# Performance work log

Hardware: AMD Instinct MI355X
Metric: run time of the kernel (lower is better)

## Reference

```python
import jax, jax.numpy as jnp
import numpy as np

VOCAB, EMB, HID, LAT, LAYERS = 32000, 512, 1024, 1024, 2
B, T = 16, 128
IN0 = EMB + HID          # layer-0 GRU input size (emb concat syn_z)
OUT_IN = HID + LAT + EMB # out-projection input (use_last_output=True)


def gru_cell(x, h, W_ih, W_hh, b_ih, b_hh):
    # PyTorch GRUCell: gates ordered [r, z, n]
    gi = x @ W_ih.T + b_ih
    gh = h @ W_hh.T + b_hh
    i_r, i_z, i_n = jnp.split(gi, 3, axis=-1)
    h_r, h_z, h_n = jnp.split(gh, 3, axis=-1)
    r = jax.nn.sigmoid(i_r + h_r)
    z = jax.nn.sigmoid(i_z + h_z)
    n = jnp.tanh(i_n + r * h_n)
    return (1.0 - z) * n + z * h


def setup_inputs() -> dict:
    key = jax.random.key(0)
    ks = jax.random.split(key, 16)
    s = 0.02
    return {
        "input_seq": jax.random.randint(ks[0], (B, T), 0, VOCAB),
        "prev_output": jnp.zeros((B, HID), jnp.float32),
        "sem_z": jax.random.normal(ks[1], (B, LAT), jnp.float32),
        "syn_z": jax.random.normal(ks[2], (B, HID), jnp.float32),
        "hidden": jnp.zeros((LAYERS, B, HID), jnp.float32),
        "emb_table": jax.random.normal(ks[3], (VOCAB, EMB), jnp.float32) * s,
        "W_ih0": jax.random.normal(ks[4], (3 * HID, IN0), jnp.float32) * s,
        "W_hh0": jax.random.normal(ks[5], (3 * HID, HID), jnp.float32) * s,
        "b_ih0": jnp.zeros((3 * HID,), jnp.float32),
        "b_hh0": jnp.zeros((3 * HID,), jnp.float32),
        "W_ih1": jax.random.normal(ks[6], (3 * HID, HID), jnp.float32) * s,
        "W_hh1": jax.random.normal(ks[7], (3 * HID, HID), jnp.float32) * s,
        "b_ih1": jnp.zeros((3 * HID,), jnp.float32),
        "b_hh1": jnp.zeros((3 * HID,), jnp.float32),
        "W_out": jax.random.normal(ks[8], (VOCAB, OUT_IN), jnp.float32) * s,
        "b_out": jnp.zeros((VOCAB,), jnp.float32),
    }


def reference(input_seq, prev_output, sem_z, syn_z, hidden, emb_table,
              W_ih0, W_hh0, b_ih0, b_hh0, W_ih1, W_hh1, b_ih1, b_hh1,
              W_out, b_out):
    # dropout=0.0 -> identity; input_feeding=False so prev_output is unused.
    embs = emb_table[input_seq]            # [B, T, E]
    embs_t = jnp.swapaxes(embs, 0, 1)      # [T, B, E]

    def step(h, emb_t):
        x = jnp.concatenate([emb_t, syn_z], axis=1)        # [B, E+H]
        h0 = gru_cell(x, h[0], W_ih0, W_hh0, b_ih0, b_hh0)  # [B, H]
        h1 = gru_cell(h0, h[1], W_ih1, W_hh1, b_ih1, b_hh1)
        pred = jnp.concatenate([h1, sem_z, emb_t], axis=1)  # [B, H+L+E]
        logits = pred @ W_out.T + b_out                     # [B, V]
        scores = jax.nn.log_softmax(logits, axis=-1)
        return jnp.stack([h0, h1]), (scores, logits)

    hidden_f, (scores, logits) = jax.lax.scan(step, hidden, embs_t)
    # scores/logits: [T, B, V]; output = last layer hidden at final step
    return scores, hidden_f, hidden_f[-1], logits
```

## Files before the change

kernel.cpp:

```cpp
#include <hip/hip_runtime.h>

typedef unsigned short u16;
typedef __attribute__((ext_vector_type(8))) short bf16x8;
typedef __attribute__((ext_vector_type(4))) float f32x4;

__device__ __forceinline__ float bf2f(u16 u) {
  union { unsigned u; float f; } v; v.u = ((unsigned)u) << 16; return v.f;
}
__device__ __forceinline__ u16 f2bf(float f) {
  union { float f; unsigned u; } v; v.f = f;
  unsigned r = v.u + 0x7FFFu + ((v.u >> 16) & 1u);
  return (u16)(r >> 16);
}

__device__ __forceinline__ f32x4 ld_sc_x4(const u16* p) {
  f32x4 r;
  asm volatile("global_load_dwordx4 %0, %1, off sc0 sc1"
               : "=v"(r) : "v"(p) : "memory");
  return r;
}
__device__ __forceinline__ float ld_sc_f32(const float* p) {
  float r;
  asm volatile("global_load_dword %0, %1, off sc0 sc1"
               : "=v"(r) : "v"(p) : "memory");
  return r;
}
__device__ __forceinline__ void st_sc_u16(u16* p, unsigned v) {
  asm volatile("global_store_short %0, %1, off sc0 sc1"
               :: "v"(p), "v"(v) : "memory");
}
__device__ __forceinline__ void st_sc_f32(float* p, float v) {
  asm volatile("global_store_dword %0, %1, off sc0 sc1"
               :: "v"(p), "v"(v) : "memory");
}
#define WAIT_VM0() asm volatile("s_waitcnt vmcnt(0)" ::: "memory")

__device__ __forceinline__ int ld_flag(const int* p) {
  return __hip_atomic_load(p, __ATOMIC_RELAXED, __HIP_MEMORY_SCOPE_AGENT);
}
__device__ __forceinline__ void st_flag(int* p, int v) {
  __hip_atomic_store(p, v, __ATOMIC_RELAXED, __HIP_MEMORY_SCOPE_AGENT);
}

constexpr size_t OFF_WCAT  = 0;
constexpr size_t OFF_WSEM  = 98304000;
constexpr size_t OFF_PART  = 98304000;
constexpr size_t OFF_H1ALL = 130000000;
constexpr size_t OFF_GI0   = 163840000;
constexpr size_t OFF_XOUT  = 189005824;
constexpr size_t OFF_H0ALL = 195297280;
constexpr size_t OFF_WIH0E = 199491584;
constexpr size_t OFF_WIH0S = 202637312;
constexpr size_t OFF_WHH0  = 208928768;
constexpr size_t OFF_WIH1  = 215220224;
constexpr size_t OFF_WHH1  = 221511680;
constexpr size_t OFF_SYNB  = 227803136;
constexpr size_t OFF_SEMB  = 228065280;
constexpr size_t OFF_BASE0 = 228327424;
constexpr size_t OFF_BASEO = 229900288;
constexpr size_t OFF_H0IBF = 246284288;
constexpr size_t OFF_H1IBF = 246317056;
constexpr size_t OFF_FLAGS = 246349824;
constexpr size_t OFF_HIDF  = 262144000;
constexpr size_t OFF_LAST  = 262275072;
constexpr size_t OFF_LOGIT = 262340608;

__global__ __launch_bounds__(256) void conv_bf16_k(
    const float* __restrict__ src, u16* __restrict__ dst,
    int rows, int cols8, int sld, int soff, int dld, int doff) {
  int t = blockIdx.x * 256 + threadIdx.x;
  if (t >= rows * cols8) return;
  int r = t / cols8, c = (t - r * cols8) * 8;
  const float* s = src + (size_t)r * sld + soff + c;
  float4 a = *(const float4*)s;
  float4 b = *(const float4*)(s + 4);
  bf16x8 o;
  o[0] = (short)f2bf(a.x); o[1] = (short)f2bf(a.y);
  o[2] = (short)f2bf(a.z); o[3] = (short)f2bf(a.w);
  o[4] = (short)f2bf(b.x); o[5] = (short)f2bf(b.y);
  o[6] = (short)f2bf(b.z); o[7] = (short)f2bf(b.w);
  *(bf16x8*)(dst + (size_t)r * dld + doff + c) = o;
}

__global__ __launch_bounds__(256) void pack_pad_bf16_k(
    const float* __restrict__ src, u16* __restrict__ dst) {
  int t = blockIdx.x * 256 + threadIdx.x;
  int row = t >> 7, c = (t & 127) * 8;
  bf16x8 o = {0, 0, 0, 0, 0, 0, 0, 0};
  if (row < 16) {
    const float* s = src + row * 1024 + c;
    float4 a = *(const float4*)s;
    float4 b = *(const float4*)(s + 4);
    o[0] = (short)f2bf(a.x); o[1] = (short)f2bf(a.y);
    o[2] = (short)f2bf(a.z); o[3] = (short)f2bf(a.w);
    o[4] = (short)f2bf(b.x); o[5] = (short)f2bf(b.y);
    o[6] = (short)f2bf(b.z); o[7] = (short)f2bf(b.w);
  }
  *(bf16x8*)(dst + (size_t)row * 1024 + c) = o;
}

__global__ __launch_bounds__(256) void gather_emb_k(
    const int* __restrict__ seq, const float* __restrict__ table,
    u16* __restrict__ xout) {
  int t0 = blockIdx.x * 256 + threadIdx.x;
  int tb = t0 >> 6, c = (t0 & 63) * 8;
  int tt = tb >> 4, b = tb & 15;
  int tok = seq[b * 128 + tt];
  const float* s = table + (size_t)tok * 512 + c;
  float4 a = *(const float4*)s;
  float4 bb = *(const float4*)(s + 4);
  bf16x8 o;
  o[0] = (short)f2bf(a.x);  o[1] = (short)f2bf(a.y);
  o[2] = (short)f2bf(a.z);  o[3] = (short)f2bf(a.w);
  o[4] = (short)f2bf(bb.x); o[5] = (short)f2bf(bb.y);
  o[6] = (short)f2bf(bb.z); o[7] = (short)f2bf(bb.w);
  *(bf16x8*)(xout + (size_t)tb * 1536 + 1024 + c) = o;
}

__global__ __launch_bounds__(256) void init_h_k(
    const float* __restrict__ hidden, u16* __restrict__ h0b,
    u16* __restrict__ h1b, int* __restrict__ flags) {
  int i = blockIdx.x * 256 + threadIdx.x;
  h0b[i] = f2bf(hidden[i]);
  h1b[i] = f2bf(hidden[16384 + i]);
  if (i < 4096) flags[i] = 0;
}

__device__ __forceinline__ void stage_tile(const u16* src, char* tile,
                                           int tid) {
  f32x4 tmp[8];
#pragma unroll
  for (int q = 0; q < 8; ++q) {
    int c = q * 256 + tid;
    int row = c >> 7, kc = c & 127;
    tmp[q] = ld_sc_x4(src + (size_t)row * 1024 + kc * 8);
  }
  WAIT_VM0();
#pragma unroll
  for (int q = 0; q < 8; ++q) {
    int c = q * 256 + tid;
    int row = c >> 7, kc = c & 127;
    int byte = (row * 2048 + kc * 16) ^ ((row & 7) << 4);
    *(bf16x8*)(tile + byte) = *(bf16x8*)&tmp[q];
  }
}

__global__ __launch_bounds__(256, 1) void gru_persist3_k(
    const float* __restrict__ hidden, const u16* __restrict__ h0i,
    const u16* __restrict__ h1i, const float* __restrict__ gi0,
    const u16* __restrict__ Whh0, const u16* __restrict__ Wih1,
    const u16* __restrict__ Whh1, const float* __restrict__ bhh0,
    const float* __restrict__ bih1, const float* __restrict__ bhh1,
    u16* __restrict__ h0all, u16* __restrict__ h1all, u16* __restrict__ xout,
    float* __restrict__ part, float* __restrict__ hidf,
    float* __restrict__ last, int* __restrict__ flags) {
  extern __shared__ char ldsb[];
  char* Ab = ldsb + 98304;
  float* Cl = (float*)(ldsb + 131072);
  const int tid = threadIdx.x, bid = blockIdx.x;
  const int wave = tid >> 6, lane = tid & 63;
  const int role = bid >> 6, lb = bid & 63, jb = lb * 16;
  int* f0 = flags, *fih = flags + 1024, *f1 = flags + 2048;

  const u16* Wsrc = role == 0 ? Whh0 : (role == 1 ? Wih1 : Whh1);
  for (int idx = tid; idx < 48 * 128; idx += 256) {
    int row = idx >> 7, c = idx & 127;
    int g = row >> 4, jj = row & 15;
    const u16* src = Wsrc + (size_t)(g * 1024 + jb + jj) * 1024 + c * 8;
    int byte = (row * 2048 + c * 16) ^ ((row & 7) << 4);
    *(bf16x8*)(ldsb + byte) = *(const bf16x8*)src;
  }

  const int eb = tid >> 4, jj = tid & 15, j = jb + jj;
  float hp = 0.f, bR = 0.f, bZ = 0.f, bN = 0.f, iR = 0.f, iZ = 0.f, iN = 0.f;
  if (role == 0) {
    hp = hidden[eb * 1024 + j];
    bR = bhh0[j]; bZ = bhh0[1024 + j]; bN = bhh0[2048 + j];
  } else if (role == 2) {
    hp = hidden[16384 + eb * 1024 + j];
    bR = bhh1[j]; bZ = bhh1[1024 + j]; bN = bhh1[2048 + j];
    iR = bih1[j]; iZ = bih1[1024 + j]; iN = bih1[2048 + j];
  }
  __syncthreads();

  const int arow = lane & 15, aq = lane >> 4;
  for (int t = 0; t < 128; ++t) {
    if (role == 0) {
      if (t > 0 && tid < 64)
        while (ld_flag(f0 + tid * 16) < t) __builtin_amdgcn_s_sleep(1);
    } else if (role == 1) {
      if (tid < 64)
        while (ld_flag(f0 + tid * 16) < t + 1) __builtin_amdgcn_s_sleep(1);
    } else {
      if (t > 0 && tid < 64)
        while (ld_flag(f1 + tid * 16) < t) __builtin_amdgcn_s_sleep(1);
    }
    __syncthreads();

    const u16* asrc;
    if (role == 0)      asrc = t ? h0all + (size_t)(t - 1) * 16384 : h0i;
    else if (role == 1) asrc = h0all + (size_t)t * 16384;
    else                asrc = t ? h1all + (size_t)(t - 1) * 16384 : h1i;
    stage_tile(asrc, Ab, tid);
    __syncthreads();

    {
      f32x4 a0 = {0.f, 0.f, 0.f, 0.f}, a1 = a0, a2 = a0;
#pragma unroll
      for (int i = 0; i < 8; ++i) {
        int ks = wave + i * 4;
        int abyte = (arow * 2048 + ks * 64 + aq * 16) ^ ((arow & 7) << 4);
        bf16x8 af = *(const bf16x8*)(Ab + abyte);
        int r0 = arow, r1 = 16 + arow, r2 = 32 + arow;
        bf16x8 b0 = *(const bf16x8*)(
            ldsb + ((r0 * 2048 + ks * 64 + aq * 16) ^ ((r0 & 7) << 4)));
        bf16x8 b1 = *(const bf16x8*)(
            ldsb + ((r1 * 2048 + ks * 64 + aq * 16) ^ ((r1 & 7) << 4)));
        bf16x8 b2 = *(const bf16x8*)(
            ldsb + ((r2 * 2048 + ks * 64 + aq * 16) ^ ((r2 & 7) << 4)));
        a0 = __builtin_amdgcn_mfma_f32_16x16x32_bf16(af, b0, a0, 0, 0, 0);
        a1 = __builtin_amdgcn_mfma_f32_16x16x32_bf16(af, b1, a1, 0, 0, 0);
        a2 = __builtin_amdgcn_mfma_f32_16x16x32_bf16(af, b2, a2, 0, 0, 0);
      }
#pragma unroll
      for (int r = 0; r < 4; ++r) {
        int ci = (aq * 4 + r) * 16 + arow;
        Cl[(0 * 4 + wave) * 256 + ci] = a0[r];
        Cl[(1 * 4 + wave) * 256 + ci] = a1[r];
        Cl[(2 * 4 + wave) * 256 + ci] = a2[r];
      }
    }
    if (role == 2 && tid == 0)
      while (ld_flag(fih + lb * 16) < t + 1) __builtin_amdgcn_s_sleep(1);
    __syncthreads();

    {
      int ci = eb * 16 + jj;
      float s0 = Cl[(0 * 4 + 0) * 256 + ci] + Cl[(0 * 4 + 1) * 256 + ci] +
                 Cl[(0 * 4 + 2) * 256 + ci] + Cl[(0 * 4 + 3) * 256 + ci];
      float s1 = Cl[(1 * 4 + 0) * 256 + ci] + Cl[(1 * 4 + 1) * 256 + ci] +
                 Cl[(1 * 4 + 2) * 256 + ci] + Cl[(1 * 4 + 3) * 256 + ci];
      float s2 = Cl[(2 * 4 + 0) * 256 + ci] + Cl[(2 * 4 + 1) * 256 + ci] +
                 Cl[(2 * 4 + 2) * 256 + ci] + Cl[(2 * 4 + 3) * 256 + ci];
      if (role == 1) {
        float* pp = part + ((size_t)t * 64 + lb) * 768 + eb * 16 + jj;
        st_sc_f32(pp, s0);
        st_sc_f32(pp + 256, s1);
        st_sc_f32(pp + 512, s2);
        WAIT_VM0();
      } else {
        float ir, iz, inn;
        if (role == 0) {
          const float* g = gi0 + ((size_t)t * 16 + eb) * 3072 + j;
          ir = g[0]; iz = g[1024]; inn = g[2048];
        } else {
          const float* pp = part + ((size_t)t * 64 + lb) * 768 + eb * 16 + jj;
          float p0 = ld_sc_f32(pp), p1 = ld_sc_f32(pp + 256),
                p2 = ld_sc_f32(pp + 512);
          WAIT_VM0();
          ir = p0 + iR; iz = p1 + iZ; inn = p2 + iN;
        }
        float r = 1.f / (1.f + __expf(-(ir + s0 + bR)));
        float z = 1.f / (1.f + __expf(-(iz + s1 + bZ)));
        float n = tanhf(inn + r * (s2 + bN));
        float hnew = (1.f - z) * n + z * hp;
        hp = hnew;
        u16 hb = f2bf(hnew);
        if (role == 0) {
          st_sc_u16(h0all + ((size_t)t * 16 + eb) * 1024 + j, (unsigned)hb);
          if (t == 127) hidf[eb * 1024 + j] = hnew;
        } else {
          st_sc_u16(h1all + ((size_t)t * 16 + eb) * 1024 + j, (unsigned)hb);
          xout[((size_t)t * 16 + eb) * 1536 + j] = hb;
          if (t == 127) {
            hidf[16384 + eb * 1024 + j] = hnew;
            last[eb * 1024 + j] = hnew;
          }
        }
        WAIT_VM0();
      }
    }
    __syncthreads();
    if (tid == 0) {
      if (role == 0)      st_flag(f0 + lb * 16, t + 1);
      else if (role == 1) st_flag(fih + lb * 16, t + 1);
      else                st_flag(f1 + lb * 16, t + 1);
    }
  }
}

template <int MODE>
__global__ __launch_bounds__(256) void gemm_bt_k(
    const u16* __restrict__ A, int lda, const u16* __restrict__ Bw, int ldb,
    float* __restrict__ C, int ldc, const float* __restrict__ add,
    int N, int K) {
  __shared__ u16 Asm_[128 * 32];
  __shared__ u16 Bsm_[128 * 32];
  const int m0 = blockIdx.x * 128, n0 = blockIdx.y * 128;
  const int tid = threadIdx.x, wave = tid >> 6, lane = tid & 63;
  const int wm = (wave >> 1) * 64, wn = (wave & 1) * 64;
  const int lrow = lane & 15, lk = (lane >> 4) * 8;
  f32x4 acc[4][4] = {};
  for (int k0 = 0; k0 < K; k0 += 32) {
    __syncthreads();
#pragma unroll
    for (int q = 0; q < 2; ++q) {
      int c = (wave * 2 + q) * 64 + lane;
      int row = c >> 2, seg = c & 3;
      const u16* src = A + (size_t)(m0 + row) * lda + k0 + seg * 8;
      u16* dst = Asm_ + (wave * 2 + q) * 512;
      __builtin_amdgcn_global_load_lds(
          (const __attribute__((address_space(1))) void*)src,
          (__attribute__((address_space(3))) void*)dst, 16, 0, 0);
    }
#pragma unroll
    for (int q = 0; q < 2; ++q) {
      int c = (wave * 2 + q) * 64 + lane;
      int row = c >> 2, seg = c & 3;
      const u16* src = Bw + (size_t)(n0 + row) * ldb + k0 + seg * 8;
      u16* dst = Bsm_ + (wave * 2 + q) * 512;
      __builtin_amdgcn_global_load_lds(
          (const __attribute__((address_space(1))) void*)src,
          (__attribute__((address_space(3))) void*)dst, 16, 0, 0);
    }
    asm volatile("s_waitcnt vmcnt(0)" ::: "memory");
    __syncthreads();
    bf16x8 af[4], bfr[4];
#pragma unroll
    for (int i = 0; i < 4; ++i) {
      af[i]  = *(const bf16x8*)(Asm_ + (wm + i * 16 + lrow) * 32 + lk);
      bfr[i] = *(const bf16x8*)(Bsm_ + (wn + i * 16 + lrow) * 32 + lk);
    }
#pragma unroll
    for (int i = 0; i < 4; ++i)
#pragma unroll
      for (int j = 0; j < 4; ++j)
        acc[i][j] = __builtin_amdgcn_mfma_f32_16x16x32_bf16(
            af[i], bfr[j], acc[i][j], 0, 0, 0);
  }
  const int lr4 = (lane >> 4) * 4;
#pragma unroll
  for (int i = 0; i < 4; ++i) {
#pragma unroll
    for (int j = 0; j < 4; ++j) {
      int gc = n0 + wn + j * 16 + lrow;
#pragma unroll
      for (int r = 0; r < 4; ++r) {
        int gr = m0 + wm + i * 16 + lr4 + r;
        float v = acc[i][j][r];
        if (MODE == 1) v += add[(gr & 15) * N + gc];
        else if (MODE == 2) v += add[gc];
        C[(size_t)gr * ldc + gc] = v;
      }
    }
  }
}

__global__ __launch_bounds__(256) void log_softmax_k(
    const float* __restrict__ logits, float* __restrict__ scores) {
  int row = blockIdx.x;
  const float* x = logits + (size_t)row * 32000;
  float* y = scores + (size_t)row * 32000;
  __shared__ float red[8];
  int tid = threadIdx.x;
  float m = -3.4e38f;
  for (int idx = tid * 4; idx < 32000; idx += 1024) {
    float4 v = *(const float4*)(x + idx);
    m = fmaxf(m, fmaxf(fmaxf(v.x, v.y), fmaxf(v.z, v.w)));
  }
  for (int off = 32; off; off >>= 1) m = fmaxf(m, __shfl_xor(m, off));
  if ((tid & 63) == 0) red[tid >> 6] = m;
  __syncthreads();
  m = fmaxf(fmaxf(red[0], red[1]), fmaxf(red[2], red[3]));
  float s = 0.f;
  for (int idx = tid * 4; idx < 32000; idx += 1024) {
    float4 v = *(const float4*)(x + idx);
    s += __expf(v.x - m) + __expf(v.y - m) + __expf(v.z - m) + __expf(v.w - m);
  }
  for (int off = 32; off; off >>= 1) s += __shfl_xor(s, off);
  if ((tid & 63) == 0) red[4 + (tid >> 6)] = s;
  __syncthreads();
  s = red[4] + red[5] + red[6] + red[7];
  float lse = m + logf(s);
  for (int idx = tid * 4; idx < 32000; idx += 1024) {
    float4 v = *(const float4*)(x + idx);
    float4 o;
    o.x = v.x - lse; o.y = v.y - lse; o.z = v.z - lse; o.w = v.w - lse;
    *(float4*)(y + idx) = o;
  }
}

extern "C" void kernel_launch(void* const* d_in, const int* in_sizes, int n_in,
                              void* d_out, int out_size, void* d_ws,
                              size_t ws_size, hipStream_t stream) {
  const int*   seq    = (const int*)d_in[0];
  const float* sem    = (const float*)d_in[2];
  const float* syn    = (const float*)d_in[3];
  const float* hidden = (const float*)d_in[4];
  const float* table  = (const float*)d_in[5];
  const float* Wih0   = (const float*)d_in[6];
  const float* Whh0   = (const float*)d_in[7];
  const float* bih0   = (const float*)d_in[8];
  const float* bhh0   = (const float*)d_in[9];
  const float* Wih1   = (const float*)d_in[10];
  const float* Whh1   = (const float*)d_in[11];
  const float* bih1   = (const float*)d_in[12];
  const float* bhh1   = (const float*)d_in[13];
  const float* Wout   = (const float*)d_in[14];
  const float* bout   = (const float*)d_in[15];

  char* base = (char*)d_out;
  float* scores = (float*)base;
  u16*   WCAT   = (u16*)(base + OFF_WCAT);
  u16*   WSEM   = (u16*)(base + OFF_WSEM);
  float* PART   = (float*)(base + OFF_PART);
  u16*   H1ALL  = (u16*)(base + OFF_H1ALL);
  float* GI0    = (float*)(base + OFF_GI0);
  u16*   XOUT   = (u16*)(base + OFF_XOUT);
  u16*   H0ALL  = (u16*)(base + OFF_H0ALL);
  u16*   WIH0E  = (u16*)(base + OFF_WIH0E);
  u16*   WIH0S  = (u16*)(base + OFF_WIH0S);
  u16*   WHH0B  = (u16*)(base + OFF_WHH0);
  u16*   WIH1B  = (u16*)(base + OFF_WIH1);
  u16*   WHH1B  = (u16*)(base + OFF_WHH1);
  u16*   SYNB   = (u16*)(base + OFF_SYNB);
  u16*   SEMB   = (u16*)(base + OFF_SEMB);
  float* BASE0  = (float*)(base + OFF_BASE0);
  float* BASEO  = (float*)(base + OFF_BASEO);
  u16*   H0IBF  = (u16*)(base + OFF_H0IBF);
  u16*   H1IBF  = (u16*)(base + OFF_H1IBF);
  int*   FLAGS  = (int*)(base + OFF_FLAGS);
  float* hidf   = (float*)(base + OFF_HIDF);
  float* last   = (float*)(base + OFF_LAST);
  float* logits = (float*)(base + OFF_LOGIT);

  conv_bf16_k<<<16000, 256, 0, stream>>>(Wout, WCAT, 32000, 128, 2560, 0, 1536, 0);
  conv_bf16_k<<<8000, 256, 0, stream>>>(Wout, WCAT, 32000, 64, 2560, 2048, 1536, 1024);
  conv_bf16_k<<<16000, 256, 0, stream>>>(Wout, WSEM, 32000, 128, 2560, 1024, 1024, 0);
  conv_bf16_k<<<768, 256, 0, stream>>>(Wih0, WIH0E, 3072, 64, 1536, 0, 512, 0);
  conv_bf16_k<<<1536, 256, 0, stream>>>(Wih0, WIH0S, 3072, 128, 1536, 512, 1024, 0);
  conv_bf16_k<<<1536, 256, 0, stream>>>(Whh0, WHH0B, 3072, 128, 1024, 0, 1024, 0);
  conv_bf16_k<<<1536, 256, 0, stream>>>(Wih1, WIH1B, 3072, 128, 1024, 0, 1024, 0);
  conv_bf16_k<<<1536, 256, 0, stream>>>(Whh1, WHH1B, 3072, 128, 1024, 0, 1024, 0);

  gather_emb_k<<<512, 256, 0, stream>>>(seq, table, XOUT);
  pack_pad_bf16_k<<<64, 256, 0, stream>>>(syn, SYNB);
  pack_pad_bf16_k<<<64, 256, 0, stream>>>(sem, SEMB);
  init_h_k<<<64, 256, 0, stream>>>(hidden, H0IBF, H1IBF, FLAGS);

  gemm_bt_k<2><<<dim3(1, 24), 256, 0, stream>>>(
      SYNB, 1024, WIH0S, 1024, BASE0, 3072, bih0, 3072, 1024);
  gemm_bt_k<2><<<dim3(1, 250), 256, 0, stream>>>(
      SEMB, 1024, WSEM, 1024, BASEO, 32000, bout, 32000, 1024);

  gemm_bt_k<1><<<dim3(16, 24), 256, 0, stream>>>(
      XOUT + 1024, 1536, WIH0E, 512, GI0, 3072, BASE0, 3072, 512);

  hipFuncSetAttribute((const void*)gru_persist3_k,
                      hipFuncAttributeMaxDynamicSharedMemorySize, 143360);
  gru_persist3_k<<<192, 256, 143360, stream>>>(
      hidden, H0IBF, H1IBF, GI0, WHH0B, WIH1B, WHH1B, bhh0, bih1, bhh1,
      H0ALL, H1ALL, XOUT, PART, hidf, last, FLAGS);

  gemm_bt_k<1><<<dim3(16, 250), 256, 0, stream>>>(
      XOUT, 1536, WCAT, 1536, logits, 32000, BASEO, 32000, 1536);

  log_softmax_k<<<2048, 256, 0, stream>>>(logits, scores);
}
```

Measured before the change: 1.277 ms.

## Load GRU A operands directly to registers, pack flags, fuse softmax passes, swizzle GEMM blocks

The persistent GRU kernel now loads the hidden-state A fragments from global memory straight into registers instead of staging them through LDS, which removes one barrier per step. It also pads the partial-sum LDS layout to avoid bank conflicts and packs the sync flags contiguously. Other changes: the three Wout conversion launches are merged into one kernel, GEMM blocks are remapped with an XCD-aware swizzle, and log_softmax computes max and sum in a single online pass. Packing the flags puts them in the same cache lines, which may add contention, and the register-loaded A path issues more redundant global reads per block.

Measured after the change: 1.580 ms. +23.7%, slower.

```diff
diff --git a/kernel.cpp b/kernel.cpp
--- a/kernel.cpp
+++ b/kernel.cpp
@@ -82,6 +82,26 @@
   *(bf16x8*)(dst + (size_t)r * dld + doff + c) = o;
 }
 
+__global__ __launch_bounds__(256) void conv_wout_k(
+    const float* __restrict__ Wout, u16* __restrict__ WCAT,
+    u16* __restrict__ WSEM) {
+  int t = blockIdx.x * 256 + threadIdx.x;
+  int r = t / 320, c = (t - r * 320) * 8;
+  const float* s = Wout + (size_t)r * 2560 + c;
+  float4 a = *(const float4*)s;
+  float4 b = *(const float4*)(s + 4);
+  bf16x8 o;
+  o[0] = (short)f2bf(a.x); o[1] = (short)f2bf(a.y);
+  o[2] = (short)f2bf(a.z); o[3] = (short)f2bf(a.w);
+  o[4] = (short)f2bf(b.x); o[5] = (short)f2bf(b.y);
+  o[6] = (short)f2bf(b.z); o[7] = (short)f2bf(b.w);
+  u16* dst;
+  if (c < 1024)      dst = WCAT + (size_t)r * 1536 + c;
+  else if (c < 2048) dst = WSEM + (size_t)r * 1024 + (c - 1024);
+  else               dst = WCAT + (size_t)r * 1536 + 1024 + (c - 2048);
+  *(bf16x8*)dst = o;
+}
+
 __global__ __launch_bounds__(256) void pack_pad_bf16_k(
     const float* __restrict__ src, u16* __restrict__ dst) {
   int t = blockIdx.x * 256 + threadIdx.x;
@@ -126,26 +146,7 @@
   if (i < 4096) flags[i] = 0;
 }
 
-__device__ __forceinline__ void stage_tile(const u16* src, char* tile,
-                                           int tid) {
-  f32x4 tmp[8];
-#pragma unroll
-  for (int q = 0; q < 8; ++q) {
-    int c = q * 256 + tid;
-    int row = c >> 7, kc = c & 127;
-    tmp[q] = ld_sc_x4(src + (size_t)row * 1024 + kc * 8);
-  }
-  WAIT_VM0();
-#pragma unroll
-  for (int q = 0; q < 8; ++q) {
-    int c = q * 256 + tid;
-    int row = c >> 7, kc = c & 127;
-    int byte = (row * 2048 + kc * 16) ^ ((row & 7) << 4);
-    *(bf16x8*)(tile + byte) = *(bf16x8*)&tmp[q];
-  }
-}
-
-__global__ __launch_bounds__(256, 1) void gru_persist3_k(
+__global__ __launch_bounds__(256, 1) void gru_persist4_k(
     const float* __restrict__ hidden, const u16* __restrict__ h0i,
     const u16* __restrict__ h1i, const float* __restrict__ gi0,
     const u16* __restrict__ Whh0, const u16* __restrict__ Wih1,
@@ -155,18 +156,19 @@
     float* __restrict__ part, float* __restrict__ hidf,
     float* __restrict__ last, int* __restrict__ flags) {
   extern __shared__ char ldsb[];
-  char* Ab = ldsb + 98304;
-  float* Cl = (float*)(ldsb + 131072);
+  float* Cl = (float*)(ldsb + 98304);
   const int tid = threadIdx.x, bid = blockIdx.x;
   const int wave = tid >> 6, lane = tid & 63;
   const int role = bid >> 6, lb = bid & 63, jb = lb * 16;
-  int* f0 = flags, *fih = flags + 1024, *f1 = flags + 2048;
+  int* f0 = flags;
+  int* fih = flags + 64;
+  int* f1 = flags + 128;
 
   const u16* Wsrc = role == 0 ? Whh0 : (role == 1 ? Wih1 : Whh1);
   for (int idx = tid; idx < 48 * 128; idx += 256) {
     int row = idx >> 7, c = idx & 127;
-    int g = row >> 4, jj = row & 15;
-    const u16* src = Wsrc + (size_t)(g * 1024 + jb + jj) * 1024 + c * 8;
+    int g = row >> 4, jj2 = row & 15;
+    const u16* src = Wsrc + (size_t)(g * 1024 + jb + jj2) * 1024 + c * 8;
     int byte = (row * 2048 + c * 16) ^ ((row & 7) << 4);
     *(bf16x8*)(ldsb + byte) = *(const bf16x8*)src;
   }
@@ -187,13 +189,13 @@
   for (int t = 0; t < 128; ++t) {
     if (role == 0) {
       if (t > 0 && tid < 64)
-        while (ld_flag(f0 + tid * 16) < t) __builtin_amdgcn_s_sleep(1);
+        while (ld_flag(f0 + tid) < t) __builtin_amdgcn_s_sleep(1);
     } else if (role == 1) {
       if (tid < 64)
-        while (ld_flag(f0 + tid * 16) < t + 1) __builtin_amdgcn_s_sleep(1);
+        while (ld_flag(f0 + tid) < t + 1) __builtin_amdgcn_s_sleep(1);
     } else {
       if (t > 0 && tid < 64)
-        while (ld_flag(f1 + tid * 16) < t) __builtin_amdgcn_s_sleep(1);
+        while (ld_flag(f1 + tid) < t) __builtin_amdgcn_s_sleep(1);
     }
     __syncthreads();
 
@@ -201,16 +203,20 @@
     if (role == 0)      asrc = t ? h0all + (size_t)(t - 1) * 16384 : h0i;
     else if (role == 1) asrc = h0all + (size_t)t * 16384;
     else                asrc = t ? h1all + (size_t)(t - 1) * 16384 : h1i;
-    stage_tile(asrc, Ab, tid);
-    __syncthreads();
+    const u16* abase = asrc + arow * 1024 + aq * 8;
+    f32x4 araw[8];
+#pragma unroll
+    for (int i = 0; i < 8; ++i)
+      araw[i] = ld_sc_x4(abase + (wave + i * 4) * 32);
+    WAIT_VM0();
+    __builtin_amdgcn_sched_barrier(0);
 
     {
       f32x4 a0 = {0.f, 0.f, 0.f, 0.f}, a1 = a0, a2 = a0;
 #pragma unroll
       for (int i = 0; i < 8; ++i) {
         int ks = wave + i * 4;
-        int abyte = (arow * 2048 + ks * 64 + aq * 16) ^ ((arow & 7) << 4);
-        bf16x8 af = *(const bf16x8*)(Ab + abyte);
+        bf16x8 af = *(bf16x8*)&araw[i];
         int r0 = arow, r1 = 16 + arow, r2 = 32 + arow;
         bf16x8 b0 = *(const bf16x8*)(
             ldsb + ((r0 * 2048 + ks * 64 + aq * 16) ^ ((r0 & 7) << 4)));
@@ -224,24 +230,24 @@
       }
 #pragma unroll
       for (int r = 0; r < 4; ++r) {
-        int ci = (aq * 4 + r) * 16 + arow;
-        Cl[(0 * 4 + wave) * 256 + ci] = a0[r];
-        Cl[(1 * 4 + wave) * 256 + ci] = a1[r];
-        Cl[(2 * 4 + wave) * 256 + ci] = a2[r];
+        int ci = (aq * 4 + r) * 16 + arow + aq * 8;
+        Cl[(0 * 4 + wave) * 288 + ci] = a0[r];
+        Cl[(1 * 4 + wave) * 288 + ci] = a1[r];
+        Cl[(2 * 4 + wave) * 288 + ci] = a2[r];
       }
     }
     if (role == 2 && tid == 0)
-      while (ld_flag(fih + lb * 16) < t + 1) __builtin_amdgcn_s_sleep(1);
+      while (ld_flag(fih + lb) < t + 1) __builtin_amdgcn_s_sleep(1);
     __syncthreads();
 
     {
-      int ci = eb * 16 + jj;
-      float s0 = Cl[(0 * 4 + 0) * 256 + ci] + Cl[(0 * 4 + 1) * 256 + ci] +
-                 Cl[(0 * 4 + 2) * 256 + ci] + Cl[(0 * 4 + 3) * 256 + ci];
-      float s1 = Cl[(1 * 4 + 0) * 256 + ci] + Cl[(1 * 4 + 1) * 256 + ci] +
-                 Cl[(1 * 4 + 2) * 256 + ci] + Cl[(1 * 4 + 3) * 256 + ci];
-      float s2 = Cl[(2 * 4 + 0) * 256 + ci] + Cl[(2 * 4 + 1) * 256 + ci] +
-                 Cl[(2 * 4 + 2) * 256 + ci] + Cl[(2 * 4 + 3) * 256 + ci];
+      int ci = eb * 16 + jj + (eb >> 2) * 8;
+      float s0 = Cl[0 * 288 + ci] + Cl[1 * 288 + ci] +
+                 Cl[2 * 288 + ci] + Cl[3 * 288 + ci];
+      float s1 = Cl[4 * 288 + ci] + Cl[5 * 288 + ci] +
+                 Cl[6 * 288 + ci] + Cl[7 * 288 + ci];
+      float s2 = Cl[8 * 288 + ci] + Cl[9 * 288 + ci] +
+                 Cl[10 * 288 + ci] + Cl[11 * 288 + ci];
       if (role == 1) {
         float* pp = part + ((size_t)t * 64 + lb) * 768 + eb * 16 + jj;
         st_sc_f32(pp, s0);
@@ -258,6 +264,7 @@
           float p0 = ld_sc_f32(pp), p1 = ld_sc_f32(pp + 256),
                 p2 = ld_sc_f32(pp + 512);
           WAIT_VM0();
+          __builtin_amdgcn_sched_barrier(0);
           ir = p0 + iR; iz = p1 + iZ; inn = p2 + iN;
         }
         float r = 1.f / (1.f + __expf(-(ir + s0 + bR)));
@@ -282,21 +289,29 @@
     }
     __syncthreads();
     if (tid == 0) {
-      if (role == 0)      st_flag(f0 + lb * 16, t + 1);
-      else if (role == 1) st_flag(fih + lb * 16, t + 1);
-      else                st_flag(f1 + lb * 16, t + 1);
-    }
-  }
-}
-
-template <int MODE>
+      if (role == 0)      st_flag(f0 + lb, t + 1);
+      else if (role == 1) st_flag(fih + lb, t + 1);
+      else                st_flag(f1 + lb, t + 1);
+    }
+  }
+}
+
+template <int MODE, bool SWZ>
 __global__ __launch_bounds__(256) void gemm_bt_k(
     const u16* __restrict__ A, int lda, const u16* __restrict__ Bw, int ldb,
     float* __restrict__ C, int ldc, const float* __restrict__ add,
     int N, int K) {
   __shared__ u16 Asm_[128 * 32];
   __shared__ u16 Bsm_[128 * 32];
-  const int m0 = blockIdx.x * 128, n0 = blockIdx.y * 128;
+  int bx = blockIdx.x, by = blockIdx.y;
+  if (SWZ) {
+    int nx = gridDim.x;
+    int orig = by * nx + bx;
+    int cpx = (nx * gridDim.y) >> 3;
+    int wg = (orig & 7) * cpx + (orig >> 3);
+    bx = wg % nx; by = wg / nx;
+  }
+  const int m0 = bx * 128, n0 = by * 128;
   const int tid = threadIdx.x, wave = tid >> 6, lane = tid & 63;
   const int wm = (wave >> 1) * 64, wn = (wave & 1) * 64;
   const int lrow = lane & 15, lk = (lane >> 4) * 8;
@@ -334,20 +349,20 @@
 #pragma unroll
     for (int i = 0; i < 4; ++i)
 #pragma unroll
-      for (int j = 0; j < 4; ++j)
-        acc[i][j] = __builtin_amdgcn_mfma_f32_16x16x32_bf16(
-            af[i], bfr[j], acc[i][j], 0, 0, 0);
+      for (int jx = 0; jx < 4; ++jx)
+        acc[i][jx] = __builtin_amdgcn_mfma_f32_16x16x32_bf16(
+            af[i], bfr[jx], acc[i][jx], 0, 0, 0);
   }
   const int lr4 = (lane >> 4) * 4;
 #pragma unroll
   for (int i = 0; i < 4; ++i) {
 #pragma unroll
-    for (int j = 0; j < 4; ++j) {
-      int gc = n0 + wn + j * 16 + lrow;
+    for (int jx = 0; jx < 4; ++jx) {
+      int gc = n0 + wn + jx * 16 + lrow;
 #pragma unroll
       for (int r = 0; r < 4; ++r) {
         int gr = m0 + wm + i * 16 + lr4 + r;
-        float v = acc[i][j][r];
+        float v = acc[i][jx][r];
         if (MODE == 1) v += add[(gr & 15) * N + gc];
         else if (MODE == 2) v += add[gc];
         C[(size_t)gr * ldc + gc] = v;
@@ -361,32 +376,34 @@
   int row = blockIdx.x;
   const float* x = logits + (size_t)row * 32000;
   float* y = scores + (size_t)row * 32000;
-  __shared__ float red[8];
+  __shared__ float redm[4], reds[4];
   int tid = threadIdx.x;
-  float m = -3.4e38f;
+  float m = -3.4e38f, s = 0.f;
   for (int idx = tid * 4; idx < 32000; idx += 1024) {
     float4 v = *(const float4*)(x + idx);
-    m = fmaxf(m, fmaxf(fmaxf(v.x, v.y), fmaxf(v.z, v.w)));
-  }
-  for (int off = 32; off; off >>= 1) m = fmaxf(m, __shfl_xor(m, off));
-  if ((tid & 63) == 0) red[tid >> 6] = m;
+    float cm = fmaxf(fmaxf(v.x, v.y), fmaxf(v.z, v.w));
+    if (cm > m) { s *= __expf(m - cm); m = cm; }
+    s += __expf(v.x - m) + __expf(v.y - m) + __expf(v.z - m) + __expf(v.w - m);
+  }
+  for (int off = 1; off < 64; off <<= 1) {
+    float mo = __shfl_xor(m, off), so = __shfl_xor(s, off);
+    float nm = fmaxf(m, mo);
+    s = s * __expf(m - nm) + so * __expf(mo - nm);
+    m = nm;
+  }
+  if ((tid & 63) == 0) { redm[tid >> 6] = m; reds[tid >> 6] = s; }
   __syncthreads();
-  m = fmaxf(fmaxf(red[0], red[1]), fmaxf(red[2], red[3]));
-  float s = 0.f;
-  for (int idx = tid * 4; idx < 32000; idx += 1024) {
-    float4 v = *(const float4*)(x + idx);
-    s += __expf(v.x - m) + __expf(v.y - m) + __expf(v.z - m) + __expf(v.w - m);
-  }
-  for (int off = 32; off; off >>= 1) s += __shfl_xor(s, off);
-  if ((tid & 63) == 0) red[4 + (tid >> 6)] = s;
-  __syncthreads();
-  s = red[4] + red[5] + red[6] + red[7];
-  float lse = m + logf(s);
-  for (int idx = tid * 4; idx < 32000; idx += 1024) {
-    float4 v = *(const float4*)(x + idx);
-    float4 o;
-    o.x = v.x - lse; o.y = v.y - lse; o.z = v.z - lse; o.w = v.w - lse;
-    *(float4*)(y + idx) = o;
+  {
+    float fm = fmaxf(fmaxf(redm[0], redm[1]), fmaxf(redm[2], redm[3]));
+    float fs = reds[0] * __expf(redm[0] - fm) + reds[1] * __expf(redm[1] - fm) +
+               reds[2] * __expf(redm[2] - fm) + reds[3] * __expf(redm[3] - fm);
+    float lse = fm + logf(fs);
+    for (int idx = tid * 4; idx < 32000; idx += 1024) {
+      float4 v = *(const float4*)(x + idx);
+      float4 o;
+      o.x = v.x - lse; o.y = v.y - lse; o.z = v.z - lse; o.w = v.w - lse;
+      *(float4*)(y + idx) = o;
+    }
   }
 }
 
@@ -434,9 +451,7 @@
   float* last   = (float*)(base + OFF_LAST);
   float* logits = (float*)(base + OFF_LOGIT);
 
-  conv_bf16_k<<<16000, 256, 0, stream>>>(Wout, WCAT, 32000, 128, 2560, 0, 1536, 0);
-  conv_bf16_k<<<8000, 256, 0, stream>>>(Wout, WCAT, 32000, 64, 2560, 2048, 1536, 1024);
-  conv_bf16_k<<<16000, 256, 0, stream>>>(Wout, WSEM, 32000, 128, 2560, 1024, 1024, 0);
+  conv_wout_k<<<40000, 256, 0, stream>>>(Wout, WCAT, WSEM);
   conv_bf16_k<<<768, 256, 0, stream>>>(Wih0, WIH0E, 3072, 64, 1536, 0, 512, 0);
   conv_bf16_k<<<1536, 256, 0, stream>>>(Wih0, WIH0S, 3072, 128, 1536, 512, 1024, 0);
   conv_bf16_k<<<1536, 256, 0, stream>>>(Whh0, WHH0B, 3072, 128, 1024, 0, 1024, 0);
@@ -448,21 +463,21 @@
   pack_pad_bf16_k<<<64, 256, 0, stream>>>(sem, SEMB);
   init_h_k<<<64, 256, 0, stream>>>(hidden, H0IBF, H1IBF, FLAGS);
 
-  gemm_bt_k<2><<<dim3(1, 24), 256, 0, stream>>>(
+  gemm_bt_k<2, false><<<dim3(1, 24), 256, 0, stream>>>(
       SYNB, 1024, WIH0S, 1024, BASE0, 3072, bih0, 3072, 1024);
-  gemm_bt_k<2><<<dim3(1, 250), 256, 0, stream>>>(
+  gemm_bt_k<2, false><<<dim3(1, 250), 256, 0, stream>>>(
       SEMB, 1024, WSEM, 1024, BASEO, 32000, bout, 32000, 1024);
 
-  gemm_bt_k<1><<<dim3(16, 24), 256, 0, stream>>>(
+  gemm_bt_k<1, true><<<dim3(16, 24), 256, 0, stream>>>(
       XOUT + 1024, 1536, WIH0E, 512, GI0, 3072, BASE0, 3072, 512);
 
-  hipFuncSetAttribute((const void*)gru_persist3_k,
-                      hipFuncAttributeMaxDynamicSharedMemorySize, 143360);
-  gru_persist3_k<<<192, 256, 143360, stream>>>(
+  hipFuncSetAttribute((const void*)gru_persist4_k,
+                      hipFuncAttributeMaxDynamicSharedMemorySize, 114688);
+  gru_persist4_k<<<192, 256, 114688, stream>>>(
       hidden, H0IBF, H1IBF, GI0, WHH0B, WIH1B, WHH1B, bhh0, bih1, bhh1,
       H0ALL, H1ALL, XOUT, PART, hidf, last, FLAGS);
 
-  gemm_bt_k<1><<<dim3(16, 250), 256, 0, stream>>>(
+  gemm_bt_k<1, true><<<dim3(16, 250), 256, 0, stream>>>(
       XOUT, 1536, WCAT, 1536, logits, 32000, BASEO, 32000, 1536);
 
   log_softmax_k<<<2048, 256, 0, stream>>>(logits, scores);
```
